# Performance work log

Measured on AMD Instinct MI355X. Metric: run time of the kernel, lower is better.

Reference implementation:

```python
import jax, jax.numpy as jnp
import numpy as np

FRAME, LATENT, HIDDEN, GATE_H, EXPERTS = 267, 32, 256, 64, 6
BATCH = 4096
IN0 = LATENT + FRAME            # 299: decoder layer-0 input (z, c)
IN1 = LATENT + HIDDEN           # 288: decoder layer-1/2 input (z, h)
OUT = FRAME                     # num_future_predictions * frame_size


def _lin(key, fan_in, fan_out):
    b = np.sqrt(1.0 / fan_in)
    return jax.random.uniform(key, (fan_in, fan_out), jnp.float32, -b, b)


def setup_inputs() -> dict:
    key = jax.random.key(0)
    ks = jax.random.split(key, 16)
    d = {
        "x": jax.random.normal(ks[0], (BATCH, FRAME), jnp.float32),
        "c": jax.random.normal(ks[1], (BATCH, FRAME), jnp.float32),
        "eps": jax.random.normal(ks[2], (BATCH, LATENT), jnp.float32),
        # encoder
        "enc_w1": _lin(ks[3], 2 * FRAME, HIDDEN), "enc_b1": jnp.zeros((HIDDEN,), jnp.float32),
        "enc_w2": _lin(ks[4], FRAME + HIDDEN, HIDDEN), "enc_b2": jnp.zeros((HIDDEN,), jnp.float32),
        "enc_wmu": _lin(ks[5], FRAME + HIDDEN, LATENT), "enc_bmu": jnp.zeros((LATENT,), jnp.float32),
        "enc_wlv": _lin(ks[6], FRAME + HIDDEN, LATENT), "enc_blv": jnp.zeros((LATENT,), jnp.float32),
        # gate MLP
        "g_w0": _lin(ks[7], IN0, GATE_H), "g_b0": jnp.zeros((GATE_H,), jnp.float32),
        "g_w1": _lin(ks[8], GATE_H, GATE_H), "g_b1": jnp.zeros((GATE_H,), jnp.float32),
        "g_w2": _lin(ks[9], GATE_H, EXPERTS), "g_b2": jnp.zeros((EXPERTS,), jnp.float32),
        # expert-mixed decoder layers (kaiming-uniform-ish init, bias 0.01)
        "w0": jax.random.uniform(ks[10], (EXPERTS, IN0, HIDDEN), jnp.float32, -np.sqrt(6.0 / IN0), np.sqrt(6.0 / IN0)),
        "b0": jnp.full((EXPERTS, HIDDEN), 0.01, jnp.float32),
        "w1": jax.random.uniform(ks[11], (EXPERTS, IN1, HIDDEN), jnp.float32, -np.sqrt(6.0 / IN1), np.sqrt(6.0 / IN1)),
        "b1": jnp.full((EXPERTS, HIDDEN), 0.01, jnp.float32),
        "w2": jax.random.uniform(ks[12], (EXPERTS, IN1, OUT), jnp.float32, -np.sqrt(6.0 / IN1), np.sqrt(6.0 / IN1)),
        "b2": jnp.full((EXPERTS, OUT), 0.01, jnp.float32),
    }
    return d


def reference(x, c, eps,
              enc_w1, enc_b1, enc_w2, enc_b2, enc_wmu, enc_bmu, enc_wlv, enc_blv,
              g_w0, g_b0, g_w1, g_b1, g_w2, g_b2,
              w0, b0, w1, b1, w2, b2):
    elu = jax.nn.elu
    # --- encoder ---
    h1 = elu(jnp.concatenate([x, c], axis=1) @ enc_w1 + enc_b1)
    h2 = elu(jnp.concatenate([x, h1], axis=1) @ enc_w2 + enc_b2)
    s = jnp.concatenate([x, h2], axis=1)
    mu = s @ enc_wmu + enc_bmu
    logvar = s @ enc_wlv + enc_blv
    z = mu + eps * jnp.exp(0.5 * logvar)
    # --- gate ---
    zc = jnp.concatenate([z, c], axis=1)
    g = elu(zc @ g_w0 + g_b0)
    g = elu(g @ g_w1 + g_b1)
    coeff = jax.nn.softmax(g @ g_w2 + g_b2, axis=1)  # [N, E]
    # --- soft-MoE decoder: blended-weight per-sample GEMMs ---
    layer = c
    for w, b, act in ((w0, b0, elu), (w1, b1, elu), (w2, b2, None)):
        inp = jnp.concatenate([z, layer], axis=1)  # [N, Din]
        # out[n,o] = sum_e coeff[n,e] * (inp[n,:] @ w[e,:,o]) + coeff[n,:] @ b[:,o]
        out = jnp.einsum('ne,ni,eio->no', coeff, inp, w) + coeff @ b
        layer = act(out) if act is not None else out
    return layer, mu, logvar
```

## Files before the change

kernel.cpp:

```cpp
#include <hip/hip_runtime.h>
#include <hip/hip_bf16.h>
#include <math.h>

#define N_BATCH 4096
#define FRAME   267
#define LATENT  32
#define HIDDEN  256
#define GATE_H  64
#define EXPERTS 6

typedef __hip_bfloat16 bf16;
typedef __bf16  bf16x8 __attribute__((ext_vector_type(8)));
typedef float   f32x4  __attribute__((ext_vector_type(4)));

__device__ __forceinline__ float eluf(float v) { return (v > 0.f) ? v : (expf(v) - 1.f); }

struct WEnt { const float* src; bf16* dst; int K, M, Mtot, mOff, Ksteps, Mtiles, cum; };
struct WTab { WEnt e[10]; int total; };

__global__ __launch_bounds__(256) void prep_kernel(
    const float* __restrict__ x, const float* __restrict__ c,
    const float* __restrict__ bmu, const float* __restrict__ blv,
    bf16* __restrict__ Axc, bf16* __restrict__ Axh1,
    bf16* __restrict__ Axh2, bf16* __restrict__ Azc,
    float* __restrict__ biasCat, WTab tab)
{
    const int tid = threadIdx.x, bid = blockIdx.x;
    if (bid < 512) {
        if (bid == 0 && tid < 64)
            biasCat[tid] = (tid < 32) ? bmu[tid] : blv[tid - 32];
        #pragma unroll 1
        for (int i = 0; i < 8; ++i) {
            const int r = bid * 8 + i;
            for (int col = tid; col < 544; col += 256) {
                const size_t o = (size_t)r * 544 + col;
                float vx = 0.f;
                if (col < FRAME)          vx = x[(size_t)r * FRAME + col];
                else if (col < 2 * FRAME) vx = c[(size_t)r * FRAME + col - FRAME];
                Axc[o] = __float2bfloat16(vx);
                if (col < FRAME) {
                    const bf16 v = __float2bfloat16(x[(size_t)r * FRAME + col]);
                    Axh1[o] = v; Axh2[o] = v;
                } else if (col >= FRAME + HIDDEN) {
                    const bf16 zv = __float2bfloat16(0.f);
                    Axh1[o] = zv; Axh2[o] = zv;
                }
                if (col >= 32 && col < 320) {
                    const float vc = (col < 32 + FRAME) ? c[(size_t)r * FRAME + col - 32] : 0.f;
                    Azc[(size_t)r * 320 + col] = __float2bfloat16(vc);
                }
            }
        }
        return;
    }
    __shared__ float tbuf[32][33];
    const int u = bid - 512;
    int i = 0;
    while (i < 9 && u >= tab.e[i + 1].cum) ++i;
    const WEnt en = tab.e[i];
    const int t = u - en.cum;
    const int perE = en.Ksteps * en.Mtiles;
    const int e = t / perE;
    const int rr = t - e * perE;
    const int mt = rr / en.Ksteps;
    const int ks = rr - mt * en.Ksteps;
    const int tx = tid & 31, ty = tid >> 5;
    const float* src = en.src + (size_t)e * en.K * en.M;
    #pragma unroll
    for (int i0 = 0; i0 < 32; i0 += 8) {
        const int k = ks * 32 + i0 + ty, m = mt * 32 + tx;
        tbuf[i0 + ty][tx] = (k < en.K && m < en.M) ? src[(size_t)k * en.M + m] : 0.f;
    }
    __syncthreads();
    bf16* dst = en.dst + ((size_t)(e * en.Ksteps + ks) * en.Mtot + en.mOff + mt * 32) * 32;
    #pragma unroll
    for (int i0 = 0; i0 < 32; i0 += 8)
        dst[(size_t)(i0 + ty) * 32 + tx] = __float2bfloat16(tbuf[tx][i0 + ty]);
}

template<int KSTEPS, int E>
__global__ __launch_bounds__(256, 4) void gemm16(
    const bf16* __restrict__ A, const bf16* __restrict__ Wt,
    const float* __restrict__ bias, const float* __restrict__ coeff,
    int M, int Mtot,
    float* __restrict__ Cf, int ldc, bf16* __restrict__ Cb, int ldcb, int act)
{
    constexpr int Kpad = KSTEPS * 32;
    constexpr int strideA = Kpad + 8;
    __shared__ bf16  sA[16 * strideA];
    __shared__ float sCo[E * 16];

    const int tid = threadIdx.x;
    const int w = tid >> 6, lane = tid & 63, ml = lane & 15, quad = lane >> 4;
    const int row0 = blockIdx.y * 16;
    const int col  = blockIdx.x * 64 + 16 * w + ml;

    if (tid < 16 * E) {
        const int e = tid >> 4, r = tid & 15;
        sCo[tid] = coeff ? coeff[(size_t)(row0 + r) * EXPERTS + e] : 1.f;
    }
    {
        const int r = tid >> 4, kt = (tid & 15) * 8;
        for (int kk = kt; kk < Kpad; kk += 128)
            *(float4*)(sA + r * strideA + kk) =
                *(const float4*)(A + (size_t)(row0 + r) * Kpad + kk);
    }
    __syncthreads();

    f32x4 acc = (f32x4){0.f, 0.f, 0.f, 0.f};
    for (int e = 0; e < E; ++e) {
        f32x4 p = (f32x4){0.f, 0.f, 0.f, 0.f};
        const bf16* wp = Wt + ((size_t)e * KSTEPS * Mtot + col) * 32 + quad * 8;
        #pragma unroll
        for (int ks = 0; ks < KSTEPS; ++ks) {
            const bf16x8 b  = *(const bf16x8*)(wp + (size_t)ks * Mtot * 32);
            const bf16x8 av = *(const bf16x8*)(sA + ml * strideA + ks * 32 + quad * 8);
            p = __builtin_amdgcn_mfma_f32_16x16x32_bf16(av, b, p, 0, 0, 0);
        }
        const float bv = (col < M) ? bias[(size_t)e * M + col] : 0.f;
        #pragma unroll
        for (int rg = 0; rg < 4; ++rg)
            acc[rg] += sCo[e * 16 + quad * 4 + rg] * (p[rg] + bv);
    }

    if (col < M) {
        #pragma unroll
        for (int rg = 0; rg < 4; ++rg) {
            const int gr = row0 + quad * 4 + rg;
            float v = acc[rg];
            if (act) v = eluf(v);
            if (Cf) Cf[(size_t)gr * ldc + col] = v;
            if (Cb) Cb[(size_t)gr * ldcb + col] = __float2bfloat16(v);
        }
    }
}

__global__ __launch_bounds__(256) void mid_kernel(
    const bf16* __restrict__ Axh2, const bf16* __restrict__ Wt_ml,
    const float* __restrict__ biasCat, const float* __restrict__ eps,
    float* __restrict__ out_mu, float* __restrict__ out_lv,
    bf16* __restrict__ Azc, bf16* __restrict__ Azd1, bf16* __restrict__ Azd2,
    const bf16* __restrict__ Wg0, const bf16* __restrict__ Wg1,
    const bf16* __restrict__ Wg2,
    const float* __restrict__ gb0, const float* __restrict__ gb1,
    const float* __restrict__ gb2, float* __restrict__ co)
{
    __shared__ bf16 sA[16 * 552];
    __shared__ char r1[8192];
    const int tid = threadIdx.x;
    const int w = tid >> 6, lane = tid & 63, ml = lane & 15, quad = lane >> 4;
    const int row0 = blockIdx.x * 16;

    float* sML = (float*)r1;
    {
        const int r = tid >> 4, kt = (tid & 15) * 8;
        for (int kk = kt; kk < 544; kk += 128)
            *(float4*)(sA + r * 552 + kk) =
                *(const float4*)(Axh2 + (size_t)(row0 + r) * 544 + kk);
    }
    __syncthreads();
    {
        const int col = 16 * w + ml;
        f32x4 p = (f32x4){0.f, 0.f, 0.f, 0.f};
        const bf16* wp = Wt_ml + (size_t)col * 32 + quad * 8;
        #pragma unroll
        for (int ks = 0; ks < 17; ++ks) {
            const bf16x8 b  = *(const bf16x8*)(wp + (size_t)ks * 64 * 32);
            const bf16x8 av = *(const bf16x8*)(sA + ml * 552 + ks * 32 + quad * 8);
            p = __builtin_amdgcn_mfma_f32_16x16x32_bf16(av, b, p, 0, 0, 0);
        }
        const float bv = biasCat[col];
        #pragma unroll
        for (int rg = 0; rg < 4; ++rg)
            sML[(quad * 4 + rg) * 64 + col] = p[rg] + bv;
    }
    __syncthreads();
    for (int i = tid; i < 16 * LATENT; i += 256) {
        const int r = i >> 5, l = i & 31;
        const float m  = sML[r * 64 + l];
        const float lv = sML[r * 64 + 32 + l];
        const int gi = (row0 + r) * LATENT + l;
        out_mu[gi] = m; out_lv[gi] = lv;
        const bf16 zb = __float2bfloat16(m + eps[gi] * expf(0.5f * lv));
        Azc [(size_t)(row0 + r) * 320 + l] = zb;
        Azd1[(size_t)(row0 + r) * 288 + l] = zb;
        Azd2[(size_t)(row0 + r) * 288 + l] = zb;
    }
    __syncthreads();
    {
        const int r = tid >> 4, kt = (tid & 15) * 8;
        for (int kk = kt; kk < 320; kk += 128)
            *(float4*)(sA + r * 328 + kk) =
                *(const float4*)(Azc + (size_t)(row0 + r) * 320 + kk);
    }
    bf16*  sG1 = (bf16*)r1;
    bf16*  sG2 = (bf16*)(r1 + 2304);
    float* sLg = (float*)(r1 + 4608);
    __syncthreads();
    {
        const int col = 16 * w + ml;
        f32x4 p = (f32x4){0.f, 0.f, 0.f, 0.f};
        const bf16* wp = Wg0 + (size_t)col * 32 + quad * 8;
        #pragma unroll
        for (int ks = 0; ks < 10; ++ks) {
            const bf16x8 b  = *(const bf16x8*)(wp + (size_t)ks * 64 * 32);
            const bf16x8 av = *(const bf16x8*)(sA + ml * 328 + ks * 32 + quad * 8);
            p = __builtin_amdgcn_mfma_f32_16x16x32_bf16(av, b, p, 0, 0, 0);
        }
        const float bv = gb0[col];
        #pragma unroll
        for (int rg = 0; rg < 4; ++rg)
            sG1[(quad * 4 + rg) * 72 + col] = __float2bfloat16(eluf(p[rg] + bv));
    }
    __syncthreads();
    {
        const int col = 16 * w + ml;
        f32x4 p = (f32x4){0.f, 0.f, 0.f, 0.f};
        const bf16* wp = Wg1 + (size_t)col * 32 + quad * 8;
        #pragma unroll
        for (int ks = 0; ks < 2; ++ks) {
            const bf16x8 b  = *(const bf16x8*)(wp + (size_t)ks * 64 * 32);
            const bf16x8 av = *(const bf16x8*)(sG1 + ml * 72 + ks * 32 + quad * 8);
            p = __builtin_amdgcn_mfma_f32_16x16x32_bf16(av, b, p, 0, 0, 0);
        }
        const float bv = gb1[col];
        #pragma unroll
        for (int rg = 0; rg < 4; ++rg)
            sG2[(quad * 4 + rg) * 72 + col] = __float2bfloat16(eluf(p[rg] + bv));
    }
    __syncthreads();
    if (w == 0) {
        f32x4 p = (f32x4){0.f, 0.f, 0.f, 0.f};
        const bf16* wp = Wg2 + (size_t)ml * 32 + quad * 8;
        #pragma unroll
        for (int ks = 0; ks < 2; ++ks) {
            const bf16x8 b  = *(const bf16x8*)(wp + (size_t)ks * 32 * 32);
            const bf16x8 av = *(const bf16x8*)(sG2 + ml * 72 + ks * 32 + quad * 8);
            p = __builtin_amdgcn_mfma_f32_16x16x32_bf16(av, b, p, 0, 0, 0);
        }
        const float bv = (ml < EXPERTS) ? gb2[ml] : 0.f;
        #pragma unroll
        for (int rg = 0; rg < 4; ++rg)
            sLg[(quad * 4 + rg) * 16 + ml] = p[rg] + bv;
    }
    __syncthreads();
    if (tid < 16) {
        float v[EXPERTS];
        float m = -1e30f;
        #pragma unroll
        for (int i = 0; i < EXPERTS; ++i) { v[i] = sLg[tid * 16 + i]; m = fmaxf(m, v[i]); }
        float s = 0.f;
        #pragma unroll
        for (int i = 0; i < EXPERTS; ++i) { v[i] = expf(v[i] - m); s += v[i]; }
        const float inv = 1.f / s;
        #pragma unroll
        for (int i = 0; i < EXPERTS; ++i)
            co[(size_t)(row0 + tid) * EXPERTS + i] = v[i] * inv;
    }
}

extern "C" void kernel_launch(void* const* d_in, const int* in_sizes, int n_in,
                              void* d_out, int out_size, void* d_ws, size_t ws_size,
                              hipStream_t stream) {
    const float* x       = (const float*)d_in[0];
    const float* c       = (const float*)d_in[1];
    const float* eps     = (const float*)d_in[2];
    const float* enc_w1  = (const float*)d_in[3];
    const float* enc_b1  = (const float*)d_in[4];
    const float* enc_w2  = (const float*)d_in[5];
    const float* enc_b2  = (const float*)d_in[6];
    const float* enc_wmu = (const float*)d_in[7];
    const float* enc_bmu = (const float*)d_in[8];
    const float* enc_wlv = (const float*)d_in[9];
    const float* enc_blv = (const float*)d_in[10];
    const float* g_w0    = (const float*)d_in[11];
    const float* g_b0    = (const float*)d_in[12];
    const float* g_w1    = (const float*)d_in[13];
    const float* g_b1    = (const float*)d_in[14];
    const float* g_w2    = (const float*)d_in[15];
    const float* g_b2    = (const float*)d_in[16];
    const float* w0      = (const float*)d_in[17];
    const float* b0      = (const float*)d_in[18];
    const float* w1      = (const float*)d_in[19];
    const float* b1      = (const float*)d_in[20];
    const float* w2      = (const float*)d_in[21];
    const float* b2      = (const float*)d_in[22];

    float* out_layer = (float*)d_out;
    float* out_mu    = out_layer + (size_t)N_BATCH * FRAME;
    float* out_lv    = out_mu    + (size_t)N_BATCH * LATENT;

    char* p = (char*)d_ws;
    float* co      = (float*)p;  p += (size_t)N_BATCH * EXPERTS * 4;
    float* biasCat = (float*)p;  p += 64 * 4;
    bf16* Axc   = (bf16*)p;      p += (size_t)N_BATCH * 544 * 2;
    bf16* Axh1  = (bf16*)p;      p += (size_t)N_BATCH * 544 * 2;
    bf16* Axh2  = (bf16*)p;      p += (size_t)N_BATCH * 544 * 2;
    bf16* Azc   = (bf16*)p;      p += (size_t)N_BATCH * 320 * 2;
    bf16* Azd1  = (bf16*)p;      p += (size_t)N_BATCH * 288 * 2;
    bf16* Azd2  = (bf16*)p;      p += (size_t)N_BATCH * 288 * 2;
    bf16* Wt_e1 = (bf16*)p;      p += (size_t)17 * 256 * 32 * 2;
    bf16* Wt_e2 = (bf16*)p;      p += (size_t)17 * 256 * 32 * 2;
    bf16* Wt_ml = (bf16*)p;      p += (size_t)17 * 64 * 32 * 2;
    bf16* Wt_g0 = (bf16*)p;      p += (size_t)10 * 64 * 32 * 2;
    bf16* Wt_g1 = (bf16*)p;      p += (size_t)2 * 64 * 32 * 2;
    bf16* Wt_g2 = (bf16*)p;      p += (size_t)2 * 32 * 32 * 2;
    bf16* Wt_w0 = (bf16*)p;      p += (size_t)EXPERTS * 10 * 256 * 32 * 2;
    bf16* Wt_w1 = (bf16*)p;      p += (size_t)EXPERTS * 9 * 256 * 32 * 2;
    bf16* Wt_w2 = (bf16*)p;      p += (size_t)EXPERTS * 9 * 320 * 32 * 2;

    WTab tab;
    int cum = 0, n = 0;
    auto add = [&](const float* src, bf16* dst, int K, int M, int Mtot, int mOff, int E) {
        int Ksteps;
        if (K == 534 || K == 523) Ksteps = 17;
        else if (K == 299) Ksteps = 10;
        else if (K == 288) Ksteps = 9;
        else Ksteps = 2;
        const int Mtiles = (M + 31) / 32;
        tab.e[n] = {src, dst, K, M, Mtot, mOff, Ksteps, Mtiles, cum};
        cum += E * Ksteps * Mtiles;
        ++n;
    };
    add(enc_w1,  Wt_e1, 534, 256, 256, 0, 1);
    add(enc_w2,  Wt_e2, 523, 256, 256, 0, 1);
    add(enc_wmu, Wt_ml, 523, 32, 64, 0, 1);
    add(enc_wlv, Wt_ml, 523, 32, 64, 32, 1);
    add(g_w0,    Wt_g0, 299, 64, 64, 0, 1);
    add(g_w1,    Wt_g1, 64, 64, 64, 0, 1);
    add(g_w2,    Wt_g2, 64, 6, 32, 0, 1);
    add(w0,      Wt_w0, 299, 256, 256, 0, EXPERTS);
    add(w1,      Wt_w1, 288, 256, 256, 0, EXPERTS);
    add(w2,      Wt_w2, 288, 267, 320, 0, EXPERTS);
    tab.total = cum;

    const dim3 blk(256);
    const int gy = N_BATCH / 16;

    prep_kernel<<<dim3(512 + cum), blk, 0, stream>>>(x, c, enc_bmu, enc_blv,
        Axc, Axh1, Axh2, Azc, biasCat, tab);

    gemm16<17, 1><<<dim3(4, gy), blk, 0, stream>>>(Axc, Wt_e1, enc_b1,
        nullptr, 256, 256, nullptr, 0, Axh1 + FRAME, 544, 1);
    gemm16<17, 1><<<dim3(4, gy), blk, 0, stream>>>(Axh1, Wt_e2, enc_b2,
        nullptr, 256, 256, nullptr, 0, Axh2 + FRAME, 544, 1);
    mid_kernel<<<dim3(gy), blk, 0, stream>>>(Axh2, Wt_ml, biasCat, eps,
        out_mu, out_lv, Azc, Azd1, Azd2, Wt_g0, Wt_g1, Wt_g2,
        g_b0, g_b1, g_b2, co);
    gemm16<10, EXPERTS><<<dim3(4, gy), blk, 0, stream>>>(Azc, Wt_w0, b0,
        co, 256, 256, nullptr, 0, Azd1 + LATENT, 288, 1);
    gemm16<9, EXPERTS><<<dim3(4, gy), blk, 0, stream>>>(Azd1, Wt_w1, b1,
        co, 256, 256, nullptr, 0, Azd2 + LATENT, 288, 1);
    gemm16<9, EXPERTS><<<dim3(5, gy), blk, 0, stream>>>(Azd2, Wt_w2, b2,
        co, FRAME, 320, out_layer, FRAME, nullptr, 0, 0);
}
```

Baseline: 202.1 us.

## Fuse encoder, gate and MoE decoder layers into one per-row-tile kernel

Replaces the chain of six GEMM/mid kernels with a single fused kernel. Each 512-thread block owns 16 batch rows and runs the encoder, mu/logvar, gate MLP, softmax and the three expert-mixed decoder layers, keeping activations in two shared-memory ping-pong buffers. Activation staging moves out of the prep kernel, which now only converts weights. This removes the global round-trips of intermediate bf16 activations and the launch gaps between kernels. The cost is only 256 blocks with heavy register use (up to 17 cached A fragments per wave). The gate stage also leaves half the waves idle, and weights are re-read per block without cross-block tile reuse.

```diff
diff --git a/kernel.cpp b/kernel.cpp
--- a/kernel.cpp
+++ b/kernel.cpp
@@ -15,50 +15,24 @@
 
 __device__ __forceinline__ float eluf(float v) { return (v > 0.f) ? v : (expf(v) - 1.f); }
 
+#define MFMA(a, b, p) __builtin_amdgcn_mfma_f32_16x16x32_bf16((a), (b), (p), 0, 0, 0)
+
 struct WEnt { const float* src; bf16* dst; int K, M, Mtot, mOff, Ksteps, Mtiles, cum; };
 struct WTab { WEnt e[10]; int total; };
 
 __global__ __launch_bounds__(256) void prep_kernel(
-    const float* __restrict__ x, const float* __restrict__ c,
     const float* __restrict__ bmu, const float* __restrict__ blv,
-    bf16* __restrict__ Axc, bf16* __restrict__ Axh1,
-    bf16* __restrict__ Axh2, bf16* __restrict__ Azc,
     float* __restrict__ biasCat, WTab tab)
 {
     const int tid = threadIdx.x, bid = blockIdx.x;
-    if (bid < 512) {
-        if (bid == 0 && tid < 64)
-            biasCat[tid] = (tid < 32) ? bmu[tid] : blv[tid - 32];
-        #pragma unroll 1
-        for (int i = 0; i < 8; ++i) {
-            const int r = bid * 8 + i;
-            for (int col = tid; col < 544; col += 256) {
-                const size_t o = (size_t)r * 544 + col;
-                float vx = 0.f;
-                if (col < FRAME)          vx = x[(size_t)r * FRAME + col];
-                else if (col < 2 * FRAME) vx = c[(size_t)r * FRAME + col - FRAME];
-                Axc[o] = __float2bfloat16(vx);
-                if (col < FRAME) {
-                    const bf16 v = __float2bfloat16(x[(size_t)r * FRAME + col]);
-                    Axh1[o] = v; Axh2[o] = v;
-                } else if (col >= FRAME + HIDDEN) {
-                    const bf16 zv = __float2bfloat16(0.f);
-                    Axh1[o] = zv; Axh2[o] = zv;
-                }
-                if (col >= 32 && col < 320) {
-                    const float vc = (col < 32 + FRAME) ? c[(size_t)r * FRAME + col - 32] : 0.f;
-                    Azc[(size_t)r * 320 + col] = __float2bfloat16(vc);
-                }
-            }
-        }
-        return;
-    }
+    if (bid == 0 && tid < 64)
+        biasCat[tid] = (tid < 32) ? bmu[tid] : blv[tid - 32];
+
     __shared__ float tbuf[32][33];
-    const int u = bid - 512;
     int i = 0;
-    while (i < 9 && u >= tab.e[i + 1].cum) ++i;
+    while (i < 9 && bid >= tab.e[i + 1].cum) ++i;
     const WEnt en = tab.e[i];
-    const int t = u - en.cum;
+    const int t = bid - en.cum;
     const int perE = en.Ksteps * en.Mtiles;
     const int e = t / perE;
     const int rr = t - e * perE;
@@ -78,96 +52,107 @@
         dst[(size_t)(i0 + ty) * 32 + tx] = __float2bfloat16(tbuf[tx][i0 + ty]);
 }
 
-template<int KSTEPS, int E>
-__global__ __launch_bounds__(256, 4) void gemm16(
-    const bf16* __restrict__ A, const bf16* __restrict__ Wt,
-    const float* __restrict__ bias, const float* __restrict__ coeff,
-    int M, int Mtot,
-    float* __restrict__ Cf, int ldc, bf16* __restrict__ Cb, int ldcb, int act)
+__global__ __launch_bounds__(512, 2) void fused_kernel(
+    const float* __restrict__ x, const float* __restrict__ c,
+    const float* __restrict__ eps,
+    const bf16* __restrict__ We1, const float* __restrict__ eb1,
+    const bf16* __restrict__ We2, const float* __restrict__ eb2,
+    const bf16* __restrict__ Wml, const float* __restrict__ biasCat,
+    const bf16* __restrict__ Wg0, const float* __restrict__ gb0,
+    const bf16* __restrict__ Wg1, const float* __restrict__ gb1,
+    const bf16* __restrict__ Wg2, const float* __restrict__ gb2,
+    const bf16* __restrict__ W0, const float* __restrict__ b0,
+    const bf16* __restrict__ W1, const float* __restrict__ b1,
+    const bf16* __restrict__ W2, const float* __restrict__ b2,
+    float* __restrict__ out_layer, float* __restrict__ out_mu,
+    float* __restrict__ out_lv)
 {
-    constexpr int Kpad = KSTEPS * 32;
-    constexpr int strideA = Kpad + 8;
-    __shared__ bf16  sA[16 * strideA];
-    __shared__ float sCo[E * 16];
-
-    const int tid = threadIdx.x;
-    const int w = tid >> 6, lane = tid & 63, ml = lane & 15, quad = lane >> 4;
-    const int row0 = blockIdx.y * 16;
-    const int col  = blockIdx.x * 64 + 16 * w + ml;
-
-    if (tid < 16 * E) {
-        const int e = tid >> 4, r = tid & 15;
-        sCo[tid] = coeff ? coeff[(size_t)(row0 + r) * EXPERTS + e] : 1.f;
-    }
-    {
-        const int r = tid >> 4, kt = (tid & 15) * 8;
-        for (int kk = kt; kk < Kpad; kk += 128)
-            *(float4*)(sA + r * strideA + kk) =
-                *(const float4*)(A + (size_t)(row0 + r) * Kpad + kk);
-    }
-    __syncthreads();
-
-    f32x4 acc = (f32x4){0.f, 0.f, 0.f, 0.f};
-    for (int e = 0; e < E; ++e) {
-        f32x4 p = (f32x4){0.f, 0.f, 0.f, 0.f};
-        const bf16* wp = Wt + ((size_t)e * KSTEPS * Mtot + col) * 32 + quad * 8;
-        #pragma unroll
-        for (int ks = 0; ks < KSTEPS; ++ks) {
-            const bf16x8 b  = *(const bf16x8*)(wp + (size_t)ks * Mtot * 32);
-            const bf16x8 av = *(const bf16x8*)(sA + ml * strideA + ks * 32 + quad * 8);
-            p = __builtin_amdgcn_mfma_f32_16x16x32_bf16(av, b, p, 0, 0, 0);
-        }
-        const float bv = (col < M) ? bias[(size_t)e * M + col] : 0.f;
-        #pragma unroll
-        for (int rg = 0; rg < 4; ++rg)
-            acc[rg] += sCo[e * 16 + quad * 4 + rg] * (p[rg] + bv);
-    }
-
-    if (col < M) {
+    __shared__ bf16  bufA[16 * 552];
+    __shared__ bf16  bufB[16 * 552];
+    __shared__ float sML[16 * 64];
+    __shared__ bf16  sG1[16 * 72];
+    __shared__ bf16  sG2[16 * 72];
+    __shared__ float sLg[16 * 16];
+    __shared__ float sCo[EXPERTS * 16];
+
+    const int tid  = threadIdx.x;
+    const int w    = tid >> 6, lane = tid & 63, ml = lane & 15, quad = lane >> 4;
+    const int row0 = blockIdx.x * 16;
+    const int r32  = tid >> 5, l32 = tid & 31;
+
+    {
+        const float* xr = x + (size_t)(row0 + r32) * FRAME;
+        const float* cr = c + (size_t)(row0 + r32) * FRAME;
+        #pragma unroll
+        for (int j = 0; j < 17; ++j) {
+            const int col = l32 + j * 32;
+            float v = 0.f;
+            if (col < FRAME)          v = xr[col];
+            else if (col < 2 * FRAME) v = cr[col - FRAME];
+            bufA[r32 * 552 + col] = __float2bfloat16(v);
+        }
+    }
+    __syncthreads();
+
+    {
+        bf16x8 av[17];
+        #pragma unroll
+        for (int ks = 0; ks < 17; ++ks)
+            av[ks] = *(const bf16x8*)(bufA + ml * 552 + ks * 32 + quad * 8);
+        const int col0 = 32 * w + ml;
+        f32x4 p0 = (f32x4){0,0,0,0}, p1 = (f32x4){0,0,0,0};
+        const bf16* wp = We1 + (size_t)col0 * 32 + quad * 8;
+        #pragma unroll
+        for (int ks = 0; ks < 17; ++ks) {
+            p0 = MFMA(av[ks], *(const bf16x8*)(wp + (size_t)ks * 256 * 32), p0);
+            p1 = MFMA(av[ks], *(const bf16x8*)(wp + (size_t)ks * 256 * 32 + 16 * 32), p1);
+        }
+        const float bv0 = eb1[col0], bv1 = eb1[col0 + 16];
         #pragma unroll
         for (int rg = 0; rg < 4; ++rg) {
-            const int gr = row0 + quad * 4 + rg;
-            float v = acc[rg];
-            if (act) v = eluf(v);
-            if (Cf) Cf[(size_t)gr * ldc + col] = v;
-            if (Cb) Cb[(size_t)gr * ldcb + col] = __float2bfloat16(v);
-        }
-    }
-}
-
-__global__ __launch_bounds__(256) void mid_kernel(
-    const bf16* __restrict__ Axh2, const bf16* __restrict__ Wt_ml,
-    const float* __restrict__ biasCat, const float* __restrict__ eps,
-    float* __restrict__ out_mu, float* __restrict__ out_lv,
-    bf16* __restrict__ Azc, bf16* __restrict__ Azd1, bf16* __restrict__ Azd2,
-    const bf16* __restrict__ Wg0, const bf16* __restrict__ Wg1,
-    const bf16* __restrict__ Wg2,
-    const float* __restrict__ gb0, const float* __restrict__ gb1,
-    const float* __restrict__ gb2, float* __restrict__ co)
-{
-    __shared__ bf16 sA[16 * 552];
-    __shared__ char r1[8192];
-    const int tid = threadIdx.x;
-    const int w = tid >> 6, lane = tid & 63, ml = lane & 15, quad = lane >> 4;
-    const int row0 = blockIdx.x * 16;
-
-    float* sML = (float*)r1;
-    {
-        const int r = tid >> 4, kt = (tid & 15) * 8;
-        for (int kk = kt; kk < 544; kk += 128)
-            *(float4*)(sA + r * 552 + kk) =
-                *(const float4*)(Axh2 + (size_t)(row0 + r) * 544 + kk);
-    }
-    __syncthreads();
-    {
+            bufB[(quad * 4 + rg) * 552 + 267 + col0]      = __float2bfloat16(eluf(p0[rg] + bv0));
+            bufB[(quad * 4 + rg) * 552 + 267 + col0 + 16] = __float2bfloat16(eluf(p1[rg] + bv1));
+        }
+        #pragma unroll
+        for (int j = 0; j < 9; ++j) {
+            const int cc = l32 + j * 32;
+            if (cc < 267) bufB[r32 * 552 + cc] = bufA[r32 * 552 + cc];
+            else          bufB[r32 * 552 + (cc - 267 + 523)] = __float2bfloat16(0.f);
+        }
+    }
+    __syncthreads();
+
+    {
+        bf16x8 av[17];
+        #pragma unroll
+        for (int ks = 0; ks < 17; ++ks)
+            av[ks] = *(const bf16x8*)(bufB + ml * 552 + ks * 32 + quad * 8);
+        const int col0 = 32 * w + ml;
+        f32x4 p0 = (f32x4){0,0,0,0}, p1 = (f32x4){0,0,0,0};
+        const bf16* wp = We2 + (size_t)col0 * 32 + quad * 8;
+        #pragma unroll
+        for (int ks = 0; ks < 17; ++ks) {
+            p0 = MFMA(av[ks], *(const bf16x8*)(wp + (size_t)ks * 256 * 32), p0);
+            p1 = MFMA(av[ks], *(const bf16x8*)(wp + (size_t)ks * 256 * 32 + 16 * 32), p1);
+        }
+        __syncthreads();
+        const float bv0 = eb2[col0], bv1 = eb2[col0 + 16];
+        #pragma unroll
+        for (int rg = 0; rg < 4; ++rg) {
+            bufB[(quad * 4 + rg) * 552 + 267 + col0]      = __float2bfloat16(eluf(p0[rg] + bv0));
+            bufB[(quad * 4 + rg) * 552 + 267 + col0 + 16] = __float2bfloat16(eluf(p1[rg] + bv1));
+        }
+    }
+    __syncthreads();
+
+    if (w < 4) {
         const int col = 16 * w + ml;
-        f32x4 p = (f32x4){0.f, 0.f, 0.f, 0.f};
-        const bf16* wp = Wt_ml + (size_t)col * 32 + quad * 8;
+        f32x4 p = (f32x4){0,0,0,0};
+        const bf16* wp = Wml + (size_t)col * 32 + quad * 8;
         #pragma unroll
         for (int ks = 0; ks < 17; ++ks) {
-            const bf16x8 b  = *(const bf16x8*)(wp + (size_t)ks * 64 * 32);
-            const bf16x8 av = *(const bf16x8*)(sA + ml * 552 + ks * 32 + quad * 8);
-            p = __builtin_amdgcn_mfma_f32_16x16x32_bf16(av, b, p, 0, 0, 0);
+            const bf16x8 av = *(const bf16x8*)(bufB + ml * 552 + ks * 32 + quad * 8);
+            p = MFMA(av, *(const bf16x8*)(wp + (size_t)ks * 64 * 32), p);
         }
         const float bv = biasCat[col];
         #pragma unroll
@@ -175,75 +160,69 @@
             sML[(quad * 4 + rg) * 64 + col] = p[rg] + bv;
     }
     __syncthreads();
-    for (int i = tid; i < 16 * LATENT; i += 256) {
-        const int r = i >> 5, l = i & 31;
-        const float m  = sML[r * 64 + l];
-        const float lv = sML[r * 64 + 32 + l];
-        const int gi = (row0 + r) * LATENT + l;
+
+    {
+        const float m  = sML[r32 * 64 + l32];
+        const float lv = sML[r32 * 64 + 32 + l32];
+        const int gi = (row0 + r32) * LATENT + l32;
         out_mu[gi] = m; out_lv[gi] = lv;
         const bf16 zb = __float2bfloat16(m + eps[gi] * expf(0.5f * lv));
-        Azc [(size_t)(row0 + r) * 320 + l] = zb;
-        Azd1[(size_t)(row0 + r) * 288 + l] = zb;
-        Azd2[(size_t)(row0 + r) * 288 + l] = zb;
-    }
-    __syncthreads();
-    {
-        const int r = tid >> 4, kt = (tid & 15) * 8;
-        for (int kk = kt; kk < 320; kk += 128)
-            *(float4*)(sA + r * 328 + kk) =
-                *(const float4*)(Azc + (size_t)(row0 + r) * 320 + kk);
-    }
-    bf16*  sG1 = (bf16*)r1;
-    bf16*  sG2 = (bf16*)(r1 + 2304);
-    float* sLg = (float*)(r1 + 4608);
-    __syncthreads();
-    {
+        bufA[r32 * 552 + l32] = zb;
+        bufB[r32 * 552 + l32] = zb;
+        #pragma unroll
+        for (int j = 0; j < 9; ++j) {
+            const int col = 32 + l32 + j * 32;
+            bf16 v = __float2bfloat16(0.f);
+            if (col < 299) v = bufA[r32 * 552 + 267 + (col - 32)];
+            bufB[r32 * 552 + col] = v;
+        }
+    }
+    __syncthreads();
+
+    if (w < 4) {
         const int col = 16 * w + ml;
-        f32x4 p = (f32x4){0.f, 0.f, 0.f, 0.f};
+        f32x4 p = (f32x4){0,0,0,0};
         const bf16* wp = Wg0 + (size_t)col * 32 + quad * 8;
         #pragma unroll
-        for (int ks = 0; ks < 10; ++ks) {
-            const bf16x8 b  = *(const bf16x8*)(wp + (size_t)ks * 64 * 32);
-            const bf16x8 av = *(const bf16x8*)(sA + ml * 328 + ks * 32 + quad * 8);
-            p = __builtin_amdgcn_mfma_f32_16x16x32_bf16(av, b, p, 0, 0, 0);
-        }
+        for (int ks = 0; ks < 10; ++ks)
+            p = MFMA(*(const bf16x8*)(bufB + ml * 552 + ks * 32 + quad * 8),
+                     *(const bf16x8*)(wp + (size_t)ks * 64 * 32), p);
         const float bv = gb0[col];
         #pragma unroll
         for (int rg = 0; rg < 4; ++rg)
             sG1[(quad * 4 + rg) * 72 + col] = __float2bfloat16(eluf(p[rg] + bv));
     }
     __syncthreads();
-    {
+
+    if (w < 4) {
         const int col = 16 * w + ml;
-        f32x4 p = (f32x4){0.f, 0.f, 0.f, 0.f};
+        f32x4 p = (f32x4){0,0,0,0};
         const bf16* wp = Wg1 + (size_t)col * 32 + quad * 8;
         #pragma unroll
-        for (int ks = 0; ks < 2; ++ks) {
-            const bf16x8 b  = *(const bf16x8*)(wp + (size_t)ks * 64 * 32);
-            const bf16x8 av = *(const bf16x8*)(sG1 + ml * 72 + ks * 32 + quad * 8);
-            p = __builtin_amdgcn_mfma_f32_16x16x32_bf16(av, b, p, 0, 0, 0);
-        }
+        for (int ks = 0; ks < 2; ++ks)
+            p = MFMA(*(const bf16x8*)(sG1 + ml * 72 + ks * 32 + quad * 8),
+                     *(const bf16x8*)(wp + (size_t)ks * 64 * 32), p);
         const float bv = gb1[col];
         #pragma unroll
         for (int rg = 0; rg < 4; ++rg)
             sG2[(quad * 4 + rg) * 72 + col] = __float2bfloat16(eluf(p[rg] + bv));
     }
     __syncthreads();
+
     if (w == 0) {
-        f32x4 p = (f32x4){0.f, 0.f, 0.f, 0.f};
+        f32x4 p = (f32x4){0,0,0,0};
         const bf16* wp = Wg2 + (size_t)ml * 32 + quad * 8;
         #pragma unroll
-        for (int ks = 0; ks < 2; ++ks) {
-            const bf16x8 b  = *(const bf16x8*)(wp + (size_t)ks * 32 * 32);
-            const bf16x8 av = *(const bf16x8*)(sG2 + ml * 72 + ks * 32 + quad * 8);
-            p = __builtin_amdgcn_mfma_f32_16x16x32_bf16(av, b, p, 0, 0, 0);
-        }
+        for (int ks = 0; ks < 2; ++ks)
+            p = MFMA(*(const bf16x8*)(sG2 + ml * 72 + ks * 32 + quad * 8),
+                     *(const bf16x8*)(wp + (size_t)ks * 32 * 32), p);
         const float bv = (ml < EXPERTS) ? gb2[ml] : 0.f;
         #pragma unroll
         for (int rg = 0; rg < 4; ++rg)
             sLg[(quad * 4 + rg) * 16 + ml] = p[rg] + bv;
     }
     __syncthreads();
+
     if (tid < 16) {
         float v[EXPERTS];
         float m = -1e30f;
@@ -254,8 +233,98 @@
         for (int i = 0; i < EXPERTS; ++i) { v[i] = expf(v[i] - m); s += v[i]; }
         const float inv = 1.f / s;
         #pragma unroll
-        for (int i = 0; i < EXPERTS; ++i)
-            co[(size_t)(row0 + tid) * EXPERTS + i] = v[i] * inv;
+        for (int i = 0; i < EXPERTS; ++i) sCo[i * 16 + tid] = v[i] * inv;
+    }
+    __syncthreads();
+
+    {
+        bf16x8 av[10];
+        #pragma unroll
+        for (int ks = 0; ks < 10; ++ks)
+            av[ks] = *(const bf16x8*)(bufB + ml * 552 + ks * 32 + quad * 8);
+        const int col0 = 32 * w + ml;
+        f32x4 acc0 = (f32x4){0,0,0,0}, acc1 = (f32x4){0,0,0,0};
+        for (int e = 0; e < EXPERTS; ++e) {
+            f32x4 p0 = (f32x4){0,0,0,0}, p1 = (f32x4){0,0,0,0};
+            const bf16* wp = W0 + ((size_t)e * 10 * 256 + col0) * 32 + quad * 8;
+            #pragma unroll
+            for (int ks = 0; ks < 10; ++ks) {
+                p0 = MFMA(av[ks], *(const bf16x8*)(wp + (size_t)ks * 256 * 32), p0);
+                p1 = MFMA(av[ks], *(const bf16x8*)(wp + (size_t)ks * 256 * 32 + 16 * 32), p1);
+            }
+            const float bv0 = b0[e * 256 + col0], bv1 = b0[e * 256 + col0 + 16];
+            #pragma unroll
+            for (int rg = 0; rg < 4; ++rg) {
+                const float cf = sCo[e * 16 + quad * 4 + rg];
+                acc0[rg] += cf * (p0[rg] + bv0);
+                acc1[rg] += cf * (p1[rg] + bv1);
+            }
+        }
+        #pragma unroll
+        for (int rg = 0; rg < 4; ++rg) {
+            bufA[(quad * 4 + rg) * 552 + 32 + col0]      = __float2bfloat16(eluf(acc0[rg]));
+            bufA[(quad * 4 + rg) * 552 + 32 + col0 + 16] = __float2bfloat16(eluf(acc1[rg]));
+        }
+    }
+    __syncthreads();
+
+    {
+        bf16x8 av[9];
+        #pragma unroll
+        for (int ks = 0; ks < 9; ++ks)
+            av[ks] = *(const bf16x8*)(bufA + ml * 552 + ks * 32 + quad * 8);
+        const int col0 = 32 * w + ml;
+        f32x4 acc0 = (f32x4){0,0,0,0}, acc1 = (f32x4){0,0,0,0};
+        for (int e = 0; e < EXPERTS; ++e) {
+            f32x4 p0 = (f32x4){0,0,0,0}, p1 = (f32x4){0,0,0,0};
+            const bf16* wp = W1 + ((size_t)e * 9 * 256 + col0) * 32 + quad * 8;
+            #pragma unroll
+            for (int ks = 0; ks < 9; ++ks) {
+                p0 = MFMA(av[ks], *(const bf16x8*)(wp + (size_t)ks * 256 * 32), p0);
+                p1 = MFMA(av[ks], *(const bf16x8*)(wp + (size_t)ks * 256 * 32 + 16 * 32), p1);
+            }
+            const float bv0 = b1[e * 256 + col0], bv1 = b1[e * 256 + col0 + 16];
+            #pragma unroll
+            for (int rg = 0; rg < 4; ++rg) {
+                const float cf = sCo[e * 16 + quad * 4 + rg];
+                acc0[rg] += cf * (p0[rg] + bv0);
+                acc1[rg] += cf * (p1[rg] + bv1);
+            }
+        }
+        __syncthreads();
+        #pragma unroll
+        for (int rg = 0; rg < 4; ++rg) {
+            bufB[(quad * 4 + rg) * 552 + 32 + col0]      = __float2bfloat16(eluf(acc0[rg]));
+            bufB[(quad * 4 + rg) * 552 + 32 + col0 + 16] = __float2bfloat16(eluf(acc1[rg]));
+        }
+    }
+    __syncthreads();
+
+    {
+        bf16x8 av[9];
+        #pragma unroll
+        for (int ks = 0; ks < 9; ++ks)
+            av[ks] = *(const bf16x8*)(bufB + ml * 552 + ks * 32 + quad * 8);
+        for (int t = w; t < 18; t += 8) {
+            const int col = 16 * t + ml;
+            f32x4 acc = (f32x4){0,0,0,0};
+            for (int e = 0; e < EXPERTS; ++e) {
+                f32x4 p = (f32x4){0,0,0,0};
+                const bf16* wp = W2 + ((size_t)e * 9 * 320 + col) * 32 + quad * 8;
+                #pragma unroll
+                for (int ks = 0; ks < 9; ++ks)
+                    p = MFMA(av[ks], *(const bf16x8*)(wp + (size_t)ks * 320 * 32), p);
+                const float bv = (col < FRAME) ? b2[e * FRAME + col] : 0.f;
+                #pragma unroll
+                for (int rg = 0; rg < 4; ++rg)
+                    acc[rg] += sCo[e * 16 + quad * 4 + rg] * (p[rg] + bv);
+            }
+            if (col < FRAME) {
+                #pragma unroll
+                for (int rg = 0; rg < 4; ++rg)
+                    out_layer[(size_t)(row0 + quad * 4 + rg) * FRAME + col] = acc[rg];
+            }
+        }
     }
 }
 
@@ -291,14 +360,7 @@
     float* out_lv    = out_mu    + (size_t)N_BATCH * LATENT;
 
     char* p = (char*)d_ws;
-    float* co      = (float*)p;  p += (size_t)N_BATCH * EXPERTS * 4;
     float* biasCat = (float*)p;  p += 64 * 4;
-    bf16* Axc   = (bf16*)p;      p += (size_t)N_BATCH * 544 * 2;
-    bf16* Axh1  = (bf16*)p;      p += (size_t)N_BATCH * 544 * 2;
-    bf16* Axh2  = (bf16*)p;      p += (size_t)N_BATCH * 544 * 2;
-    bf16* Azc   = (bf16*)p;      p += (size_t)N_BATCH * 320 * 2;
-    bf16* Azd1  = (bf16*)p;      p += (size_t)N_BATCH * 288 * 2;
-    bf16* Azd2  = (bf16*)p;      p += (size_t)N_BATCH * 288 * 2;
     bf16* Wt_e1 = (bf16*)p;      p += (size_t)17 * 256 * 32 * 2;
     bf16* Wt_e2 = (bf16*)p;      p += (size_t)17 * 256 * 32 * 2;
     bf16* Wt_ml = (bf16*)p;      p += (size_t)17 * 64 * 32 * 2;
@@ -334,23 +396,12 @@
     add(w2,      Wt_w2, 288, 267, 320, 0, EXPERTS);
     tab.total = cum;
 
-    const dim3 blk(256);
-    const int gy = N_BATCH / 16;
-
-    prep_kernel<<<dim3(512 + cum), blk, 0, stream>>>(x, c, enc_bmu, enc_blv,
-        Axc, Axh1, Axh2, Azc, biasCat, tab);
-
-    gemm16<17, 1><<<dim3(4, gy), blk, 0, stream>>>(Axc, Wt_e1, enc_b1,
-        nullptr, 256, 256, nullptr, 0, Axh1 + FRAME, 544, 1);
-    gemm16<17, 1><<<dim3(4, gy), blk, 0, stream>>>(Axh1, Wt_e2, enc_b2,
-        nullptr, 256, 256, nullptr, 0, Axh2 + FRAME, 544, 1);
-    mid_kernel<<<dim3(gy), blk, 0, stream>>>(Axh2, Wt_ml, biasCat, eps,
-        out_mu, out_lv, Azc, Azd1, Azd2, Wt_g0, Wt_g1, Wt_g2,
-        g_b0, g_b1, g_b2, co);
-    gemm16<10, EXPERTS><<<dim3(4, gy), blk, 0, stream>>>(Azc, Wt_w0, b0,
-        co, 256, 256, nullptr, 0, Azd1 + LATENT, 288, 1);
-    gemm16<9, EXPERTS><<<dim3(4, gy), blk, 0, stream>>>(Azd1, Wt_w1, b1,
-        co, 256, 256, nullptr, 0, Azd2 + LATENT, 288, 1);
-    gemm16<9, EXPERTS><<<dim3(5, gy), blk, 0, stream>>>(Azd2, Wt_w2, b2,
-        co, FRAME, 320, out_layer, FRAME, nullptr, 0, 0);
+    prep_kernel<<<dim3(cum), dim3(256), 0, stream>>>(enc_bmu, enc_blv, biasCat, tab);
+
+    fused_kernel<<<dim3(N_BATCH / 16), dim3(512), 0, stream>>>(
+        x, c, eps,
+        Wt_e1, enc_b1, Wt_e2, enc_b2, Wt_ml, biasCat,
+        Wt_g0, g_b0, Wt_g1, g_b1, Wt_g2, g_b2,
+        Wt_w0, b0, Wt_w1, b1, Wt_w2, b2,
+        out_layer, out_mu, out_lv);
 }
```

New measurement: 187.5 us. -7.2%, faster.
